# Kernel optimization log

Measured on AMD Instinct MI355X. Metric: run time of the kernel, lower is better.

The kernel has to match this reference:

```python
import jax, jax.numpy as jnp
import numpy as np
from jax import lax

KS = 3  # kernel_size


def setup_inputs() -> dict:
    key = jax.random.key(0)
    k1, k2, k3 = jax.random.split(key, 3)
    B, D, C_IN, F = 4, 96, 16, 16
    feat = jax.random.normal(k1, (B, D, D, D, C_IN), dtype=jnp.float32)
    index = jax.random.randint(k2, (B, D, D, D), 0, 2, dtype=jnp.int32)
    # glorot-style scale for w [c_in * ks^3, filters]
    fan_in = C_IN * KS ** 3
    w = jax.random.normal(k3, (fan_in, F), dtype=jnp.float32) * jnp.float32(np.sqrt(2.0 / (fan_in + F)))
    b = jnp.zeros((F,), dtype=jnp.float32)
    return {"feat": feat, "index": index, "w": w, "b": b}


def reference(feat, index, w, b):
    # SparseConv: for every voxel where index != 0, gather the ks^3 neighborhood
    # (out-of-bounds neighbors read as zero), flatten to [N, ks^3 * C_in],
    # matmul with w, add b, and scatter back (zeros elsewhere).
    # The meshgrid('ij') offset order followed by reshape([-1, ks^3 * C_in])
    # makes w row index = ((dx*ks + dy)*ks + dz)*C_in + c_in, i.e. exactly a
    # dense 3-D cross-correlation kernel w.reshape(ks, ks, ks, C_in, F) with
    # SAME zero padding; the scatter_nd equals masking the output by index != 0.
    c_in = feat.shape[-1]
    filters = w.shape[-1]
    w_conv = w.reshape(KS, KS, KS, c_in, filters)  # DHWIO
    out = lax.conv_general_dilated(
        feat, w_conv,
        window_strides=(1, 1, 1),
        padding="SAME",
        dimension_numbers=("NDHWC", "DHWIO", "NDHWC"),
    ) + b
    mask = (index != 0)[..., None]  # [B, X, Y, Z, 1]
    return jnp.where(mask, out, jnp.zeros((), dtype=out.dtype))
```

## Files before the change

kernel.cpp:

```cpp
#include <hip/hip_runtime.h>

#define DSZ 96
#define CIN 16
#define NF  16
#define NXT (DSZ / 8)
#define NYT (DSZ / 8)
#define NZT (DSZ / 16)

typedef __attribute__((ext_vector_type(8))) short short8;
typedef __attribute__((ext_vector_type(4))) float f32x4;

union I4S8 { int4 i; short8 s; };

__global__ void pack_w(const float* __restrict__ w, short* __restrict__ wpack) {
  const int t = threadIdx.x >> 6;
  const int l = threadIdx.x & 63;
  const int tap = 2 * t + (l >> 5);
  const int cib = ((l >> 4) & 1) * 8;
  const int f = l & 15;
  short v[8];
#pragma unroll
  for (int j = 0; j < 8; ++j) {
    float x = (tap <= 26) ? w[(tap * 16 + cib + j) * 16 + f] : 0.0f;
    unsigned u = __float_as_uint(x);
    u = (u + 0x7FFFu + ((u >> 16) & 1u)) >> 16;
    v[j] = (short)u;
  }
  short8 s;
#pragma unroll
  for (int j = 0; j < 8; ++j) s[j] = v[j];
  reinterpret_cast<short8*>(wpack)[t * 64 + l] = s;
}

__global__ __launch_bounds__(512, 4) void conv_mfma_lds(
    const float* __restrict__ feat, const int* __restrict__ index,
    const float* __restrict__ bias, const short8* __restrict__ wpack,
    float* __restrict__ out) {
  __shared__ short smem[100 * 18 * 16];

  const int tid = threadIdx.x;
  const int lane = tid & 63;
  const int wid = tid >> 6;

  const int d = blockIdx.x;
  int L = (d & 7) * 432 + (d >> 3);
  const int yt = L % NYT;  L /= NYT;
  const int zt = L % NZT;  L /= NZT;
  const int xt = L % NXT;
  const int b  = L / NXT;
  const int x0 = xt * 8, y0 = yt * 8, z0 = zt * 16;

  short8 bw[14];
#pragma unroll
  for (int t = 0; t < 14; ++t) bw[t] = wpack[t * 64 + lane];

  for (int it = tid; it < 1800; it += 512) {
    const int col = it / 18;
    const int zp  = it - col * 18;
    const int colx = col / 10;
    const int coly = col - colx * 10;
    const int gx = x0 + colx - 1, gy = y0 + coly - 1, gz = z0 + zp - 1;
    const bool ok = ((unsigned)gx < (unsigned)DSZ) &
                    ((unsigned)gy < (unsigned)DSZ) &
                    ((unsigned)gz < (unsigned)DSZ);
    const long off = ok ? ((long)(((b * DSZ + gx) * DSZ + gy) * DSZ + gz) * CIN) : 0;
    const float4* p = reinterpret_cast<const float4*>(feat + off);
    float4 q0 = p[0], q1 = p[1], q2 = p[2], q3 = p[3];
    unsigned m0 = __builtin_amdgcn_perm(__float_as_uint(q0.y), __float_as_uint(q0.x), 0x07060302u);
    unsigned m1 = __builtin_amdgcn_perm(__float_as_uint(q0.w), __float_as_uint(q0.z), 0x07060302u);
    unsigned m2 = __builtin_amdgcn_perm(__float_as_uint(q1.y), __float_as_uint(q1.x), 0x07060302u);
    unsigned m3 = __builtin_amdgcn_perm(__float_as_uint(q1.w), __float_as_uint(q1.z), 0x07060302u);
    unsigned m4 = __builtin_amdgcn_perm(__float_as_uint(q2.y), __float_as_uint(q2.x), 0x07060302u);
    unsigned m5 = __builtin_amdgcn_perm(__float_as_uint(q2.w), __float_as_uint(q2.z), 0x07060302u);
    unsigned m6 = __builtin_amdgcn_perm(__float_as_uint(q3.y), __float_as_uint(q3.x), 0x07060302u);
    unsigned m7 = __builtin_amdgcn_perm(__float_as_uint(q3.w), __float_as_uint(q3.z), 0x07060302u);
    if (!ok) { m0 = m1 = m2 = m3 = m4 = m5 = m6 = m7 = 0u; }
    const int byte0 = (col * 576 + zp * 32) ^ ((zp & 4) << 2);
    *reinterpret_cast<int4*>((char*)smem + byte0)        = make_int4(m0, m1, m2, m3);
    *reinterpret_cast<int4*>((char*)smem + (byte0 ^ 16)) = make_int4(m4, m5, m6, m7);
  }

  const int cx = wid;
  const int tp = lane >> 5;
  int pre[3];
#pragma unroll
  for (int dz = 0; dz < 3; ++dz) {
    const int zp = (lane & 15) + dz;
    pre[dz] = (zp * 32 + (lane & 16)) ^ ((zp & 4) << 2);
  }
  int laddr[14];
#pragma unroll
  for (int t = 0; t < 14; ++t) {
    const int tapA = 2 * t;
    const int tapB = (2 * t + 1 <= 26) ? (2 * t + 1) : 26;
    const int aA = ((cx + tapA / 9) * 10 + (tapA / 3) % 3) * 576 + pre[tapA % 3];
    const int aB = ((cx + tapB / 9) * 10 + (tapB / 3) % 3) * 576 + pre[tapB % 3];
    laddr[t] = tp ? aB : aA;
  }

  const int fq = lane & 15, hq = lane >> 4;
  const float bf = bias[fq];
  const char* smb = (const char*)smem;

  const int vbase0 = ((b * DSZ + (x0 + cx)) * DSZ + y0) * DSZ + z0;
  const int* ip = index + vbase0 + hq * 4;
  float* op = out + (long)(vbase0 + hq * 4) * NF + fq;

  __syncthreads();

#pragma unroll 2
  for (int cy = 0; cy < 8; ++cy) {
    f32x4 acc0 = {0.f, 0.f, 0.f, 0.f};
    f32x4 acc1 = {0.f, 0.f, 0.f, 0.f};
#pragma unroll
    for (int t = 0; t < 14; ++t) {
      I4S8 u;
      u.i = *reinterpret_cast<const int4*>(smb + laddr[t] + cy * 576);
      if (t & 1)
        acc1 = __builtin_amdgcn_mfma_f32_16x16x32_bf16(u.s, bw[t], acc1, 0, 0, 0);
      else
        acc0 = __builtin_amdgcn_mfma_f32_16x16x32_bf16(u.s, bw[t], acc0, 0, 0, 0);
    }
    const int4 iv = *reinterpret_cast<const int4*>(ip);
    op[0 * NF] = iv.x ? (acc0[0] + acc1[0] + bf) : 0.0f;
    op[1 * NF] = iv.y ? (acc0[1] + acc1[1] + bf) : 0.0f;
    op[2 * NF] = iv.z ? (acc0[2] + acc1[2] + bf) : 0.0f;
    op[3 * NF] = iv.w ? (acc0[3] + acc1[3] + bf) : 0.0f;
    ip += DSZ;
    op += (long)DSZ * NF;
  }
}

__global__ __launch_bounds__(256) void sparse_conv_f32(
    const float* __restrict__ feat, const int* __restrict__ index,
    const float* __restrict__ w, const float* __restrict__ bias,
    float* __restrict__ out) {
  const int v = blockIdx.x * 256 + threadIdx.x;
  const int z = v % DSZ;
  int t = v / DSZ;
  const int y = t % DSZ; t /= DSZ;
  const int x = t % DSZ;
  const int bb = t / DSZ;
  float acc[NF];
#pragma unroll
  for (int f = 0; f < NF; ++f) acc[f] = bias[f];
  const bool active = (index[v] != 0);
#pragma unroll 1
  for (int kx = -1; kx <= 1; ++kx) {
    const int xx = x + kx;
    const bool okx = ((unsigned)xx < (unsigned)DSZ);
#pragma unroll 1
    for (int ky = -1; ky <= 1; ++ky) {
      const int yy = y + ky;
      const bool oky = okx && ((unsigned)yy < (unsigned)DSZ);
#pragma unroll 1
      for (int kz = -1; kz <= 1; ++kz) {
        const int zz = z + kz;
        const bool ok = oky && ((unsigned)zz < (unsigned)DSZ);
        const long long off = ((((long long)bb * DSZ + xx) * DSZ + yy) * DSZ + zz) * CIN;
        float4 q0, q1, q2, q3;
        if (ok) {
          const float4* fp = reinterpret_cast<const float4*>(feat + off);
          q0 = fp[0]; q1 = fp[1]; q2 = fp[2]; q3 = fp[3];
        } else {
          q0 = q1 = q2 = q3 = make_float4(0.f, 0.f, 0.f, 0.f);
        }
        const float fv[CIN] = {q0.x, q0.y, q0.z, q0.w, q1.x, q1.y, q1.z, q1.w,
                               q2.x, q2.y, q2.z, q2.w, q3.x, q3.y, q3.z, q3.w};
        const float* wr = w + ((((kx + 1) * 3 + (ky + 1)) * 3 + (kz + 1)) * CIN) * NF;
#pragma unroll
        for (int ci = 0; ci < CIN; ++ci) {
          const float fvv = fv[ci];
#pragma unroll
          for (int f = 0; f < NF; ++f) acc[f] = fmaf(fvv, wr[ci * NF + f], acc[f]);
        }
      }
    }
  }
  float4* op = reinterpret_cast<float4*>(out + (long long)v * NF);
  if (active) {
    op[0] = make_float4(acc[0], acc[1], acc[2], acc[3]);
    op[1] = make_float4(acc[4], acc[5], acc[6], acc[7]);
    op[2] = make_float4(acc[8], acc[9], acc[10], acc[11]);
    op[3] = make_float4(acc[12], acc[13], acc[14], acc[15]);
  } else {
    const float4 z4 = make_float4(0.f, 0.f, 0.f, 0.f);
    op[0] = z4; op[1] = z4; op[2] = z4; op[3] = z4;
  }
}

extern "C" void kernel_launch(void* const* d_in, const int* in_sizes, int n_in,
                              void* d_out, int out_size, void* d_ws, size_t ws_size,
                              hipStream_t stream) {
  const float* feat  = (const float*)d_in[0];
  const int*   index = (const int*)d_in[1];
  const float* w     = (const float*)d_in[2];
  const float* bias  = (const float*)d_in[3];
  float*       out   = (float*)d_out;

  const int nvox = in_sizes[1];

  if (ws_size < 14 * 64 * 8 * sizeof(short)) {
    sparse_conv_f32<<<nvox / 256, 256, 0, stream>>>(feat, index, w, bias, out);
    return;
  }

  short* wpack = (short*)d_ws;
  pack_w<<<1, 14 * 64, 0, stream>>>(w, wpack);

  const int blocks = 4 * NXT * NYT * NZT;
  conv_mfma_lds<<<blocks, 512, 0, stream>>>(feat, index, bias,
                                            (const short8*)wpack, out);
}
```

Before: 131.4 us.

## Reuse each LDS A-fragment across multiple y-outputs with register accumulators

```diff
diff --git a/kernel.cpp b/kernel.cpp
--- a/kernel.cpp
+++ b/kernel.cpp
@@ -3,9 +3,9 @@
 #define DSZ 96
 #define CIN 16
 #define NF  16
-#define NXT (DSZ / 8)
-#define NYT (DSZ / 8)
-#define NZT (DSZ / 16)
+#define NXT 12
+#define NYT 12
+#define NZT 6
 
 typedef __attribute__((ext_vector_type(8))) short short8;
 typedef __attribute__((ext_vector_type(4))) float f32x4;
@@ -13,15 +13,25 @@
 union I4S8 { int4 i; short8 s; };
 
 __global__ void pack_w(const float* __restrict__ w, short* __restrict__ wpack) {
-  const int t = threadIdx.x >> 6;
-  const int l = threadIdx.x & 63;
-  const int tap = 2 * t + (l >> 5);
+  const int g = blockIdx.x;
+  const int l = threadIdx.x;
+  const int tp = l >> 5;
   const int cib = ((l >> 4) & 1) * 8;
   const int f = l & 15;
+  int tap;
+  bool zero = false;
+  if (g < 9) {
+    tap = g * 3 + tp;
+  } else if (g < 12) {
+    tap = ((g - 9) * 3 + tp) * 3 + 2;
+  } else {
+    tap = ((g - 12) * 3 + 2) * 3 + 2;
+    zero = (tp == 1);
+  }
   short v[8];
 #pragma unroll
   for (int j = 0; j < 8; ++j) {
-    float x = (tap <= 26) ? w[(tap * 16 + cib + j) * 16 + f] : 0.0f;
+    float x = zero ? 0.0f : w[(tap * 16 + cib + j) * 16 + f];
     unsigned u = __float_as_uint(x);
     u = (u + 0x7FFFu + ((u >> 16) & 1u)) >> 16;
     v[j] = (short)u;
@@ -29,14 +39,14 @@
   short8 s;
 #pragma unroll
   for (int j = 0; j < 8; ++j) s[j] = v[j];
-  reinterpret_cast<short8*>(wpack)[t * 64 + l] = s;
+  reinterpret_cast<short8*>(wpack)[g * 64 + l] = s;
 }
 
 __global__ __launch_bounds__(512, 4) void conv_mfma_lds(
     const float* __restrict__ feat, const int* __restrict__ index,
     const float* __restrict__ bias, const short8* __restrict__ wpack,
     float* __restrict__ out) {
-  __shared__ short smem[100 * 18 * 16];
+  __shared__ short smem[101 * 288];
 
   const int tid = threadIdx.x;
   const int lane = tid & 63;
@@ -50,9 +60,9 @@
   const int b  = L / NXT;
   const int x0 = xt * 8, y0 = yt * 8, z0 = zt * 16;
 
-  short8 bw[14];
-#pragma unroll
-  for (int t = 0; t < 14; ++t) bw[t] = wpack[t * 64 + lane];
+  short8 bw[15];
+#pragma unroll
+  for (int t = 0; t < 15; ++t) bw[t] = wpack[t * 64 + lane];
 
   for (int it = tid; it < 1800; it += 512) {
     const int col = it / 18;
@@ -79,55 +89,60 @@
     *reinterpret_cast<int4*>((char*)smem + byte0)        = make_int4(m0, m1, m2, m3);
     *reinterpret_cast<int4*>((char*)smem + (byte0 ^ 16)) = make_int4(m4, m5, m6, m7);
   }
-
+  if (tid < 36)
+    *reinterpret_cast<int4*>((char*)smem + 100 * 576 + tid * 16) =
+        make_int4(0, 0, 0, 0);
+
+  const int r = lane & 15, h16v = lane & 16, tp = lane >> 5;
+  const int zp01 = r + tp;
+  const int pre01 = (zp01 * 32 + h16v) ^ ((zp01 & 4) << 2);
+  const int zpm = r + 2;
+  const int preMx = ((zpm * 32 + h16v) ^ ((zpm & 4) << 2)) + tp * 576;
   const int cx = wid;
-  const int tp = lane >> 5;
-  int pre[3];
-#pragma unroll
-  for (int dz = 0; dz < 3; ++dz) {
-    const int zp = (lane & 15) + dz;
-    pre[dz] = (zp * 32 + (lane & 16)) ^ ((zp & 4) << 2);
-  }
-  int laddr[14];
-#pragma unroll
-  for (int t = 0; t < 14; ++t) {
-    const int tapA = 2 * t;
-    const int tapB = (2 * t + 1 <= 26) ? (2 * t + 1) : 26;
-    const int aA = ((cx + tapA / 9) * 10 + (tapA / 3) % 3) * 576 + pre[tapA % 3];
-    const int aB = ((cx + tapB / 9) * 10 + (tapB / 3) % 3) * 576 + pre[tapB % 3];
-    laddr[t] = tp ? aB : aA;
-  }
+  const int base01 = pre01 + cx * 5760;
+  const int baseMx = preMx + cx * 5760;
 
   const int fq = lane & 15, hq = lane >> 4;
   const float bf = bias[fq];
   const char* smb = (const char*)smem;
 
+  f32x4 acc[8];
+#pragma unroll
+  for (int cy = 0; cy < 8; ++cy) acc[cy] = f32x4{0.f, 0.f, 0.f, 0.f};
+
+  __syncthreads();
+
+#pragma unroll
+  for (int dx = 0; dx < 3; ++dx) {
+#pragma unroll
+    for (int yc = 0; yc < 10; ++yc) {
+      const int o = dx * 5760 + yc * 576;
+      I4S8 a01, amx;
+      a01.i = *reinterpret_cast<const int4*>(smb + base01 + o);
+      amx.i = *reinterpret_cast<const int4*>(smb + baseMx + o);
+      if (yc <= 7)
+        acc[yc]     = __builtin_amdgcn_mfma_f32_16x16x32_bf16(a01.s, bw[dx * 3 + 0], acc[yc], 0, 0, 0);
+      if (yc >= 1 && yc <= 8)
+        acc[yc - 1] = __builtin_amdgcn_mfma_f32_16x16x32_bf16(a01.s, bw[dx * 3 + 1], acc[yc - 1], 0, 0, 0);
+      if (yc >= 2)
+        acc[yc - 2] = __builtin_amdgcn_mfma_f32_16x16x32_bf16(a01.s, bw[dx * 3 + 2], acc[yc - 2], 0, 0, 0);
+      if (yc <= 7)
+        acc[yc]     = __builtin_amdgcn_mfma_f32_16x16x32_bf16(amx.s, bw[9 + dx],  acc[yc], 0, 0, 0);
+      if (yc >= 2)
+        acc[yc - 2] = __builtin_amdgcn_mfma_f32_16x16x32_bf16(amx.s, bw[12 + dx], acc[yc - 2], 0, 0, 0);
+    }
+  }
+
   const int vbase0 = ((b * DSZ + (x0 + cx)) * DSZ + y0) * DSZ + z0;
-  const int* ip = index + vbase0 + hq * 4;
-  float* op = out + (long)(vbase0 + hq * 4) * NF + fq;
-
-  __syncthreads();
-
-#pragma unroll 2
+#pragma unroll
   for (int cy = 0; cy < 8; ++cy) {
-    f32x4 acc0 = {0.f, 0.f, 0.f, 0.f};
-    f32x4 acc1 = {0.f, 0.f, 0.f, 0.f};
-#pragma unroll
-    for (int t = 0; t < 14; ++t) {
-      I4S8 u;
-      u.i = *reinterpret_cast<const int4*>(smb + laddr[t] + cy * 576);
-      if (t & 1)
-        acc1 = __builtin_amdgcn_mfma_f32_16x16x32_bf16(u.s, bw[t], acc1, 0, 0, 0);
-      else
-        acc0 = __builtin_amdgcn_mfma_f32_16x16x32_bf16(u.s, bw[t], acc0, 0, 0, 0);
-    }
-    const int4 iv = *reinterpret_cast<const int4*>(ip);
-    op[0 * NF] = iv.x ? (acc0[0] + acc1[0] + bf) : 0.0f;
-    op[1 * NF] = iv.y ? (acc0[1] + acc1[1] + bf) : 0.0f;
-    op[2 * NF] = iv.z ? (acc0[2] + acc1[2] + bf) : 0.0f;
-    op[3 * NF] = iv.w ? (acc0[3] + acc1[3] + bf) : 0.0f;
-    ip += DSZ;
-    op += (long)DSZ * NF;
+    const int vb = vbase0 + cy * DSZ;
+    const int4 iv = *reinterpret_cast<const int4*>(index + vb + hq * 4);
+    float* op = out + (long)(vb + hq * 4) * NF + fq;
+    op[0 * NF] = iv.x ? (acc[cy][0] + bf) : 0.0f;
+    op[1 * NF] = iv.y ? (acc[cy][1] + bf) : 0.0f;
+    op[2 * NF] = iv.z ? (acc[cy][2] + bf) : 0.0f;
+    op[3 * NF] = iv.w ? (acc[cy][3] + bf) : 0.0f;
   }
 }
 
@@ -200,13 +215,13 @@
 
   const int nvox = in_sizes[1];
 
-  if (ws_size < 14 * 64 * 8 * sizeof(short)) {
+  if (ws_size < 15 * 64 * 8 * sizeof(short)) {
     sparse_conv_f32<<<nvox / 256, 256, 0, stream>>>(feat, index, w, bias, out);
     return;
   }
 
   short* wpack = (short*)d_ws;
-  pack_w<<<1, 14 * 64, 0, stream>>>(w, wpack);
+  pack_w<<<15, 64, 0, stream>>>(w, wpack);
 
   const int blocks = 4 * NXT * NYT * NZT;
   conv_mfma_lds<<<blocks, 512, 0, stream>>>(feat, index, bias,
```

Result: slower. 195.2 us (+48.5%).

## Process three z-tiles per block with register-staged prefetch overlapping MFMA compute

Applied to the files above, without the earlier changes.

```diff
diff --git a/kernel.cpp b/kernel.cpp
--- a/kernel.cpp
+++ b/kernel.cpp
@@ -3,9 +3,6 @@
 #define DSZ 96
 #define CIN 16
 #define NF  16
-#define NXT (DSZ / 8)
-#define NYT (DSZ / 8)
-#define NZT (DSZ / 16)
 
 typedef __attribute__((ext_vector_type(8))) short short8;
 typedef __attribute__((ext_vector_type(4))) float f32x4;
@@ -32,53 +29,76 @@
   reinterpret_cast<short8*>(wpack)[t * 64 + l] = s;
 }
 
-__global__ __launch_bounds__(512, 4) void conv_mfma_lds(
+__global__ __launch_bounds__(512, 2) void conv_mfma_col(
     const float* __restrict__ feat, const int* __restrict__ index,
     const float* __restrict__ bias, const short8* __restrict__ wpack,
     float* __restrict__ out) {
-  __shared__ short smem[100 * 18 * 16];
+  __shared__ short smem[100 * 288];
 
   const int tid = threadIdx.x;
   const int lane = tid & 63;
   const int wid = tid >> 6;
 
   const int d = blockIdx.x;
-  int L = (d & 7) * 432 + (d >> 3);
-  const int yt = L % NYT;  L /= NYT;
-  const int zt = L % NZT;  L /= NZT;
-  const int xt = L % NXT;
-  const int b  = L / NXT;
-  const int x0 = xt * 8, y0 = yt * 8, z0 = zt * 16;
+  int L = (d & 7) * 144 + (d >> 3);
+  const int yt = L % 12;  L /= 12;
+  const int xt = L % 12;  L /= 12;
+  const int zc = L & 1;
+  const int b  = L >> 1;
+  const int x0 = xt * 8, y0 = yt * 8, zc0 = zc * 48;
 
   short8 bw[14];
 #pragma unroll
   for (int t = 0; t < 14; ++t) bw[t] = wpack[t * 64 + lane];
 
-  for (int it = tid; it < 1800; it += 512) {
-    const int col = it / 18;
-    const int zp  = it - col * 18;
-    const int colx = col / 10;
-    const int coly = col - colx * 10;
-    const int gx = x0 + colx - 1, gy = y0 + coly - 1, gz = z0 + zp - 1;
-    const bool ok = ((unsigned)gx < (unsigned)DSZ) &
-                    ((unsigned)gy < (unsigned)DSZ) &
-                    ((unsigned)gz < (unsigned)DSZ);
-    const long off = ok ? ((long)(((b * DSZ + gx) * DSZ + gy) * DSZ + gz) * CIN) : 0;
-    const float4* p = reinterpret_cast<const float4*>(feat + off);
-    float4 q0 = p[0], q1 = p[1], q2 = p[2], q3 = p[3];
-    unsigned m0 = __builtin_amdgcn_perm(__float_as_uint(q0.y), __float_as_uint(q0.x), 0x07060302u);
-    unsigned m1 = __builtin_amdgcn_perm(__float_as_uint(q0.w), __float_as_uint(q0.z), 0x07060302u);
-    unsigned m2 = __builtin_amdgcn_perm(__float_as_uint(q1.y), __float_as_uint(q1.x), 0x07060302u);
-    unsigned m3 = __builtin_amdgcn_perm(__float_as_uint(q1.w), __float_as_uint(q1.z), 0x07060302u);
-    unsigned m4 = __builtin_amdgcn_perm(__float_as_uint(q2.y), __float_as_uint(q2.x), 0x07060302u);
-    unsigned m5 = __builtin_amdgcn_perm(__float_as_uint(q2.w), __float_as_uint(q2.z), 0x07060302u);
-    unsigned m6 = __builtin_amdgcn_perm(__float_as_uint(q3.y), __float_as_uint(q3.x), 0x07060302u);
-    unsigned m7 = __builtin_amdgcn_perm(__float_as_uint(q3.w), __float_as_uint(q3.z), 0x07060302u);
-    if (!ok) { m0 = m1 = m2 = m3 = m4 = m5 = m6 = m7 = 0u; }
-    const int byte0 = (col * 576 + zp * 32) ^ ((zp & 4) << 2);
-    *reinterpret_cast<int4*>((char*)smem + byte0)        = make_int4(m0, m1, m2, m3);
-    *reinterpret_cast<int4*>((char*)smem + (byte0 ^ 16)) = make_int4(m4, m5, m6, m7);
-  }
+  float4 sq[4][4];
+  int sok[4];
+
+  auto stage_load = [&](int z0) {
+#pragma unroll
+    for (int k = 0; k < 4; ++k) {
+      const int i = tid + k * 512;
+      const int col = i / 18;
+      const int zp  = i - col * 18;
+      const int colx = col / 10, coly = col - colx * 10;
+      const int gx = x0 + colx - 1, gy = y0 + coly - 1, gz = z0 + zp - 1;
+      const bool ok = (i < 1800) & ((unsigned)gx < (unsigned)DSZ) &
+                      ((unsigned)gy < (unsigned)DSZ) &
+                      ((unsigned)gz < (unsigned)DSZ);
+      sok[k] = ok;
+      if (ok) {
+        const float4* p = reinterpret_cast<const float4*>(
+            feat + (long)(((b * DSZ + gx) * DSZ + gy) * DSZ + gz) * CIN);
+        sq[k][0] = p[0];
+        sq[k][1] = p[1];
+        sq[k][2] = p[2];
+        sq[k][3] = p[3];
+      }
+    }
+  };
+
+  auto stage_write = [&]() {
+#pragma unroll
+    for (int k = 0; k < 4; ++k) {
+      const int i = tid + k * 512;
+      if (i < 1800) {
+        const int col = i / 18;
+        const int zp  = i - col * 18;
+        unsigned m0 = __builtin_amdgcn_perm(__float_as_uint(sq[k][0].y), __float_as_uint(sq[k][0].x), 0x07060302u);
+        unsigned m1 = __builtin_amdgcn_perm(__float_as_uint(sq[k][0].w), __float_as_uint(sq[k][0].z), 0x07060302u);
+        unsigned m2 = __builtin_amdgcn_perm(__float_as_uint(sq[k][1].y), __float_as_uint(sq[k][1].x), 0x07060302u);
+        unsigned m3 = __builtin_amdgcn_perm(__float_as_uint(sq[k][1].w), __float_as_uint(sq[k][1].z), 0x07060302u);
+        unsigned m4 = __builtin_amdgcn_perm(__float_as_uint(sq[k][2].y), __float_as_uint(sq[k][2].x), 0x07060302u);
+        unsigned m5 = __builtin_amdgcn_perm(__float_as_uint(sq[k][2].w), __float_as_uint(sq[k][2].z), 0x07060302u);
+        unsigned m6 = __builtin_amdgcn_perm(__float_as_uint(sq[k][3].y), __float_as_uint(sq[k][3].x), 0x07060302u);
+        unsigned m7 = __builtin_amdgcn_perm(__float_as_uint(sq[k][3].w), __float_as_uint(sq[k][3].z), 0x07060302u);
+        if (!sok[k]) { m0 = m1 = m2 = m3 = m4 = m5 = m6 = m7 = 0u; }
+        const int byte0 = (col * 576 + zp * 32) ^ ((zp & 4) << 2);
+        *reinterpret_cast<int4*>((char*)smem + byte0)        = make_int4(m0, m1, m2, m3);
+        *reinterpret_cast<int4*>((char*)smem + (byte0 ^ 16)) = make_int4(m4, m5, m6, m7);
+      }
+    }
+  };
 
   const int cx = wid;
   const int tp = lane >> 5;
@@ -101,34 +121,58 @@
   const int fq = lane & 15, hq = lane >> 4;
   const float bf = bias[fq];
   const char* smb = (const char*)smem;
-
-  const int vbase0 = ((b * DSZ + (x0 + cx)) * DSZ + y0) * DSZ + z0;
-  const int* ip = index + vbase0 + hq * 4;
-  float* op = out + (long)(vbase0 + hq * 4) * NF + fq;
-
-  __syncthreads();
-
+  const int vcol = ((b * DSZ + (x0 + cx)) * DSZ + y0) * DSZ + hq * 4;
+
+  int4 iv[8];
+
+  auto load_iv = [&](int z0) {
+#pragma unroll
+    for (int cy = 0; cy < 8; ++cy)
+      iv[cy] = *reinterpret_cast<const int4*>(index + vcol + cy * DSZ + z0);
+  };
+
+  auto compute_main = [&](int z0) {
 #pragma unroll 2
-  for (int cy = 0; cy < 8; ++cy) {
-    f32x4 acc0 = {0.f, 0.f, 0.f, 0.f};
-    f32x4 acc1 = {0.f, 0.f, 0.f, 0.f};
-#pragma unroll
-    for (int t = 0; t < 14; ++t) {
-      I4S8 u;
-      u.i = *reinterpret_cast<const int4*>(smb + laddr[t] + cy * 576);
-      if (t & 1)
-        acc1 = __builtin_amdgcn_mfma_f32_16x16x32_bf16(u.s, bw[t], acc1, 0, 0, 0);
-      else
-        acc0 = __builtin_amdgcn_mfma_f32_16x16x32_bf16(u.s, bw[t], acc0, 0, 0, 0);
-    }
-    const int4 iv = *reinterpret_cast<const int4*>(ip);
-    op[0 * NF] = iv.x ? (acc0[0] + acc1[0] + bf) : 0.0f;
-    op[1 * NF] = iv.y ? (acc0[1] + acc1[1] + bf) : 0.0f;
-    op[2 * NF] = iv.z ? (acc0[2] + acc1[2] + bf) : 0.0f;
-    op[3 * NF] = iv.w ? (acc0[3] + acc1[3] + bf) : 0.0f;
-    ip += DSZ;
-    op += (long)DSZ * NF;
-  }
+    for (int cy = 0; cy < 8; ++cy) {
+      f32x4 acc0 = {0.f, 0.f, 0.f, 0.f};
+      f32x4 acc1 = {0.f, 0.f, 0.f, 0.f};
+#pragma unroll
+      for (int t = 0; t < 14; ++t) {
+        I4S8 u;
+        u.i = *reinterpret_cast<const int4*>(smb + laddr[t] + cy * 576);
+        if (t & 1)
+          acc1 = __builtin_amdgcn_mfma_f32_16x16x32_bf16(u.s, bw[t], acc1, 0, 0, 0);
+        else
+          acc0 = __builtin_amdgcn_mfma_f32_16x16x32_bf16(u.s, bw[t], acc0, 0, 0, 0);
+      }
+      float* op = out + (long)(vcol + cy * DSZ + z0) * NF + fq;
+      op[0 * NF] = iv[cy].x ? (acc0[0] + acc1[0] + bf) : 0.0f;
+      op[1 * NF] = iv[cy].y ? (acc0[1] + acc1[1] + bf) : 0.0f;
+      op[2 * NF] = iv[cy].z ? (acc0[2] + acc1[2] + bf) : 0.0f;
+      op[3 * NF] = iv[cy].w ? (acc0[3] + acc1[3] + bf) : 0.0f;
+    }
+  };
+
+  stage_load(zc0);
+  stage_write();
+  __syncthreads();
+
+  load_iv(zc0);
+  stage_load(zc0 + 16);
+  compute_main(zc0);
+  __syncthreads();
+  stage_write();
+  __syncthreads();
+
+  load_iv(zc0 + 16);
+  stage_load(zc0 + 32);
+  compute_main(zc0 + 16);
+  __syncthreads();
+  stage_write();
+  __syncthreads();
+
+  load_iv(zc0 + 32);
+  compute_main(zc0 + 32);
 }
 
 __global__ __launch_bounds__(256) void sparse_conv_f32(
@@ -208,7 +252,7 @@
   short* wpack = (short*)d_ws;
   pack_w<<<1, 14 * 64, 0, stream>>>(w, wpack);
 
-  const int blocks = 4 * NXT * NYT * NZT;
-  conv_mfma_lds<<<blocks, 512, 0, stream>>>(feat, index, bias,
+  const int blocks = 4 * 2 * 12 * 12;
+  conv_mfma_col<<<blocks, 512, 0, stream>>>(feat, index, bias,
                                             (const short8*)wpack, out);
 }
```

Result: slower. 222.2 us (+69.1%).
